# Kernel tuning notes

Measured on AMD Instinct MI355X. Metric: run time of the kernel, lower is better.

Reference implementation:

```python
import jax, jax.numpy as jnp
import numpy as np

# ---- module hyperparameters (match init_kwargs) ----
SPATIAL = (32, 64)          # token grid, N = 32*64 = 2048
D_MODEL = 1024
N_HEADS = 16
HEAD_DIM = D_MODEL // N_HEADS  # 64
THETA = 10000.0
XPOS_SCALE_BASE = SPATIAL[0] * 2  # 64


def _rope_tables():
    """ND rotary (xpos) tables, lucidrains-style.
    Each spatial axis gets head_dim//ndim rotary channels; frequencies are
    interleave-repeated (r=2) to pair with rotate_half. Returns cos, sin,
    xpos scale, each [N, HEAD_DIM] float32."""
    nd = len(SPATIAL)
    dpa = HEAD_DIM // nd  # dims per axis (32)
    freqs_axes, scale_axes = [], []
    for size in SPATIAL:
        inv_freq = 1.0 / (THETA ** (np.arange(0, dpa, 2, dtype=np.float64) / dpa))
        t = np.arange(size, dtype=np.float64)
        f = np.repeat(t[:, None] * inv_freq[None, :], 2, axis=-1)        # [size, dpa]
        sbase = (np.arange(0, dpa, 2, dtype=np.float64) + 0.4 * dpa) / (1.4 * dpa)
        power = (t - size // 2) / XPOS_SCALE_BASE
        sc = np.repeat(sbase[None, :] ** power[:, None], 2, axis=-1)     # [size, dpa]
        freqs_axes.append(f)
        scale_axes.append(sc)
    # broadcast each axis table over the full grid, concat along channel dim
    def grid_concat(tabs):
        parts = []
        for i, tab in enumerate(tabs):
            shp = [1] * nd + [dpa]
            shp[i] = SPATIAL[i]
            parts.append(np.broadcast_to(tab.reshape(shp), tuple(SPATIAL) + (dpa,)))
        return np.concatenate(parts, axis=-1).reshape(-1, HEAD_DIM)  # [N, HEAD_DIM]
    freqs = grid_concat(freqs_axes)
    xscale = grid_concat(scale_axes)
    return (jnp.asarray(np.cos(freqs), jnp.float32),
            jnp.asarray(np.sin(freqs), jnp.float32),
            jnp.asarray(xscale, jnp.float32))


def _rotate_half(x):
    # pairwise rotation: (x1, x2) -> (-x2, x1), interleaved layout
    x = x.reshape(*x.shape[:-1], -1, 2)
    x1, x2 = x[..., 0], x[..., 1]
    return jnp.stack((-x2, x1), axis=-1).reshape(*x.shape[:-2], -1)


def setup_inputs() -> dict:
    key = jax.random.key(0)
    ks = jax.random.split(key, 3)
    B, N = 2, SPATIAL[0] * SPATIAL[1]
    x = jax.random.normal(ks[0], (B, N, D_MODEL), dtype=jnp.float32)
    w_qkv = jax.random.normal(ks[1], (D_MODEL, 3 * D_MODEL), dtype=jnp.float32) * 0.02
    b_qkv = jnp.zeros((3 * D_MODEL,), jnp.float32)
    w_proj = jax.random.normal(ks[2], (D_MODEL, D_MODEL), dtype=jnp.float32) * 0.02
    b_proj = jnp.zeros((D_MODEL,), jnp.float32)
    return {"x": x, "w_qkv": w_qkv, "b_qkv": b_qkv, "w_proj": w_proj, "b_proj": b_proj}


def reference(x, w_qkv, b_qkv, w_proj, b_proj):
    B, N, C = x.shape
    scale = HEAD_DIM ** -0.5
    qkv = (x @ w_qkv + b_qkv).reshape(B, N, 3, N_HEADS, HEAD_DIM)
    qkv = qkv.transpose(2, 0, 3, 1, 4)  # [3, B, H, N, D]
    q, k, v = qkv[0], qkv[1], qkv[2]
    cos, sin, xs = _rope_tables()       # [N, D], broadcast over B,H
    q = (q * cos + _rotate_half(q) * sin) * xs
    k = (k * cos + _rotate_half(k) * sin) / xs
    attn = jax.nn.softmax(jnp.einsum('bhnd,bhmd->bhnm', q, k) * scale, axis=-1)
    out = jnp.einsum('bhnm,bhmd->bhnd', attn, v)
    out = out.transpose(0, 2, 1, 3).reshape(B, N, C)
    return out @ w_proj + b_proj
```

## Files before the change

kernel.cpp:

```cpp
#include <hip/hip_runtime.h>
#include <math.h>

typedef __attribute__((ext_vector_type(8))) _Float16 f16x8;
typedef __attribute__((ext_vector_type(4))) _Float16 f16x4;
typedef __attribute__((ext_vector_type(4))) float f32x4;

#define MFMAH(a, b, c) __builtin_amdgcn_mfma_f32_16x16x32_f16((a), (b), (c), 0, 0, 0)

#define QSCALE 0.18033688011112042f
#define SOFF 4.328085122666891f


__global__ void prep_kernel(const float* __restrict__ x, const float* __restrict__ w_qkv,
                            const float* __restrict__ w_proj, _Float16* __restrict__ xb,
                            _Float16* __restrict__ wq, _Float16* __restrict__ wp,
                            float* __restrict__ ct, float* __restrict__ st,
                            float* __restrict__ xt) {
    const int b = blockIdx.x, tid = threadIdx.x;
    if (b < 16384) {
        int i = b * 256 + tid;
        xb[i] = (_Float16)x[i];
    } else if (b < 28672) {
        int i = (b - 16384) * 256 + tid;
        int c = i >> 10, r = i & 1023;
        wq[i] = (_Float16)w_qkv[(size_t)r * 3072 + c];
    } else if (b < 32768) {
        int i = (b - 28672) * 256 + tid;
        int c = i >> 10, r = i & 1023;
        wp[i] = (_Float16)w_proj[(size_t)r * 1024 + c];
    } else {
        int i = (b - 32768) * 256 + tid;
        int n = i >> 6, d = i & 63;
        int gi = n >> 6, gj = n & 63;
        int axis = d >> 5;
        int p = (d & 31) >> 1;
        float t = axis ? (float)gj : (float)gi;
        float half = axis ? 32.0f : 16.0f;
        float inv_freq = powf(10000.0f, -(float)p * (1.0f / 16.0f));
        float fr = t * inv_freq;
        float sbase = (2.0f * p + 12.8f) / 44.8f;
        float xs = powf(sbase, (t - half) * (1.0f / 64.0f));
        ct[i] = cosf(fr);
        st[i] = sinf(fr);
        xt[i] = xs;
    }
}

#define LDK 40

__global__ __launch_bounds__(256) void gemm_qkv_kernel(
    const _Float16* __restrict__ A_g, const _Float16* __restrict__ B_g,
    const float* __restrict__ bias, const float* __restrict__ ctab,
    const float* __restrict__ stab, const float* __restrict__ xtab,
    _Float16* __restrict__ qb, _Float16* __restrict__ kb, _Float16* __restrict__ vt) {
    __shared__ __align__(16) _Float16 Asm[128 * LDK];
    __shared__ __align__(16) _Float16 Bsm[128 * LDK];

    const int tid = threadIdx.x;
    const int lane = tid & 63, wave = tid >> 6;
    const int quad = lane >> 4, l16 = lane & 15;
    const int wm = wave >> 1, wn = wave & 1;
    const int m0 = blockIdx.x * 128, n0 = blockIdx.y * 128;

    f32x4 zero = {0.f, 0.f, 0.f, 0.f};
    f32x4 acc[4][4];
#pragma unroll
    for (int i = 0; i < 4; ++i)
#pragma unroll
        for (int j = 0; j < 4; ++j) acc[i][j] = zero;

    const int r0 = tid >> 2, o0 = (tid & 3) << 3;
    const size_t ab = (size_t)m0 * 1024;
    const size_t bb = (size_t)n0 * 1024;

    f16x8 pa0 = *(const f16x8*)&A_g[ab + (size_t)r0 * 1024 + o0];
    f16x8 pa1 = *(const f16x8*)&A_g[ab + (size_t)(r0 + 64) * 1024 + o0];
    f16x8 pb0 = *(const f16x8*)&B_g[bb + (size_t)r0 * 1024 + o0];
    f16x8 pb1 = *(const f16x8*)&B_g[bb + (size_t)(r0 + 64) * 1024 + o0];

    for (int k0 = 0; k0 < 1024; k0 += 32) {
        __syncthreads();
        *(f16x8*)&Asm[r0 * LDK + o0] = pa0;
        *(f16x8*)&Asm[(r0 + 64) * LDK + o0] = pa1;
        *(f16x8*)&Bsm[r0 * LDK + o0] = pb0;
        *(f16x8*)&Bsm[(r0 + 64) * LDK + o0] = pb1;
        __syncthreads();

        if (k0 + 32 < 1024) {
            const int kn = k0 + 32;
            pa0 = *(const f16x8*)&A_g[ab + kn + (size_t)r0 * 1024 + o0];
            pa1 = *(const f16x8*)&A_g[ab + kn + (size_t)(r0 + 64) * 1024 + o0];
            pb0 = *(const f16x8*)&B_g[bb + kn + (size_t)r0 * 1024 + o0];
            pb1 = *(const f16x8*)&B_g[bb + kn + (size_t)(r0 + 64) * 1024 + o0];
        }

        f16x8 af[4], bf[4];
#pragma unroll
        for (int i = 0; i < 4; ++i) {
            af[i] = *(const f16x8*)&Asm[(wm * 64 + i * 16 + l16) * LDK + quad * 8];
            bf[i] = *(const f16x8*)&Bsm[(wn * 64 + i * 16 + l16) * LDK + quad * 8];
        }
#pragma unroll
        for (int i = 0; i < 4; ++i)
#pragma unroll
            for (int j = 0; j < 4; ++j) acc[i][j] = MFMAH(af[i], bf[j], acc[i][j]);
    }

    float bj[4];
#pragma unroll
    for (int j = 0; j < 4; ++j) bj[j] = bias[n0 + wn * 64 + j * 16 + l16];

    if (n0 < 2048) {
#pragma unroll
        for (int i = 0; i < 4; ++i) {
#pragma unroll
            for (int r = 0; r < 4; ++r) {
                const int row = m0 + wm * 64 + i * 16 + quad * 4 + r;
                const int b = row >> 11, nrow = row & 2047;
#pragma unroll
                for (int j = 0; j < 4; ++j) {
                    const int col = n0 + wn * 64 + j * 16 + l16;
                    float v = acc[i][j][r] + bj[j];
                    float partner = __shfl_xor(v, 1);
                    const int hh = (col >> 6) & 15;
                    const int d = col & 63;
                    const size_t o = ((size_t)(b * 16 + hh) * 2048 + nrow) * 64 + d;
                    float rh = (d & 1) ? partner : -partner;
                    const int ti = nrow * 64 + d;
                    float rv = v * ctab[ti] + rh * stab[ti];
                    float xs = xtab[ti];
                    if (col < 1024)
                        qb[o] = (_Float16)(rv * xs * QSCALE);
                    else
                        kb[o] = (_Float16)(rv / xs);
                }
            }
        }
    } else {
#pragma unroll
        for (int i = 0; i < 4; ++i) {
            const int row = m0 + wm * 64 + i * 16 + quad * 4;
            const int b = row >> 11, nrow = row & 2047;
#pragma unroll
            for (int j = 0; j < 4; ++j) {
                const int col = n0 + wn * 64 + j * 16 + l16;
                const int hh = (col >> 6) & 15;
                const int d = col & 63;
                f16x4 pv4;
#pragma unroll
                for (int r = 0; r < 4; ++r) pv4[r] = (_Float16)(acc[i][j][r] + bj[j]);
                *(f16x4*)&vt[((size_t)(b * 16 + hh) * 64 + d) * 2048 + nrow] = pv4;
            }
        }
    }
}

__global__ __launch_bounds__(256) void gemm_proj_kernel(
    const _Float16* __restrict__ A_g, const _Float16* __restrict__ B_g,
    const float* __restrict__ bias, float* __restrict__ out) {
    __shared__ __align__(16) _Float16 Asm[128 * LDK];
    __shared__ __align__(16) _Float16 Bsm[64 * LDK];

    const int tid = threadIdx.x;
    const int lane = tid & 63, wave = tid >> 6;
    const int quad = lane >> 4, l16 = lane & 15;
    const int wm = wave >> 1, wn = wave & 1;
    const int m0 = blockIdx.x * 128, n0 = blockIdx.y * 64;

    f32x4 zero = {0.f, 0.f, 0.f, 0.f};
    f32x4 acc[4][2];
#pragma unroll
    for (int i = 0; i < 4; ++i)
#pragma unroll
        for (int j = 0; j < 2; ++j) acc[i][j] = zero;

    const int r0 = tid >> 2, o0 = (tid & 3) << 3;
    const size_t ab = (size_t)m0 * 1024;
    const size_t bb = (size_t)n0 * 1024;

    f16x8 pa0 = *(const f16x8*)&A_g[ab + (size_t)r0 * 1024 + o0];
    f16x8 pa1 = *(const f16x8*)&A_g[ab + (size_t)(r0 + 64) * 1024 + o0];
    f16x8 pb0 = *(const f16x8*)&B_g[bb + (size_t)r0 * 1024 + o0];

    for (int k0 = 0; k0 < 1024; k0 += 32) {
        __syncthreads();
        *(f16x8*)&Asm[r0 * LDK + o0] = pa0;
        *(f16x8*)&Asm[(r0 + 64) * LDK + o0] = pa1;
        *(f16x8*)&Bsm[r0 * LDK + o0] = pb0;
        __syncthreads();

        if (k0 + 32 < 1024) {
            const int kn = k0 + 32;
            pa0 = *(const f16x8*)&A_g[ab + kn + (size_t)r0 * 1024 + o0];
            pa1 = *(const f16x8*)&A_g[ab + kn + (size_t)(r0 + 64) * 1024 + o0];
            pb0 = *(const f16x8*)&B_g[bb + kn + (size_t)r0 * 1024 + o0];
        }

        f16x8 af[4], bf[2];
#pragma unroll
        for (int i = 0; i < 4; ++i)
            af[i] = *(const f16x8*)&Asm[(wm * 64 + i * 16 + l16) * LDK + quad * 8];
#pragma unroll
        for (int j = 0; j < 2; ++j)
            bf[j] = *(const f16x8*)&Bsm[(wn * 32 + j * 16 + l16) * LDK + quad * 8];
#pragma unroll
        for (int i = 0; i < 4; ++i)
#pragma unroll
            for (int j = 0; j < 2; ++j) acc[i][j] = MFMAH(af[i], bf[j], acc[i][j]);
    }

    float bj[2];
#pragma unroll
    for (int j = 0; j < 2; ++j) bj[j] = bias[n0 + wn * 32 + j * 16 + l16];
#pragma unroll
    for (int i = 0; i < 4; ++i)
#pragma unroll
        for (int r = 0; r < 4; ++r) {
            const int row = m0 + wm * 64 + i * 16 + quad * 4 + r;
#pragma unroll
            for (int j = 0; j < 2; ++j) {
                const int col = n0 + wn * 32 + j * 16 + l16;
                out[(size_t)row * 1024 + col] = acc[i][j][r] + bj[j];
            }
        }
}

#define KLD 72
#define PLD 72

__global__ __launch_bounds__(256) void attn_kernel(
    const _Float16* __restrict__ qb, const _Float16* __restrict__ kb,
    const _Float16* __restrict__ vt, _Float16* __restrict__ ao) {
    __shared__ __align__(16) _Float16 Ksm0[64 * KLD], Ksm1[64 * KLD];
    __shared__ __align__(16) _Float16 Vsm0[64 * KLD], Vsm1[64 * KLD];
    __shared__ __align__(16) _Float16 Psm[4 * 32 * PLD];

    const int tid = threadIdx.x;
    const int lane = tid & 63, wave = tid >> 6;
    const int quad = lane >> 4, l16 = lane & 15;
    const int bh = blockIdx.x & 31, qt = blockIdx.x >> 5;
    const size_t base = (size_t)bh * 2048 * 64;
    const int qrow0 = qt * 128 + wave * 32;

    f16x8 qf[2][2];
#pragma unroll
    for (int rg = 0; rg < 2; ++rg) {
        qf[rg][0] = *(const f16x8*)&qb[base + (size_t)(qrow0 + rg * 16 + l16) * 64 + quad * 8];
        qf[rg][1] = *(const f16x8*)&qb[base + (size_t)(qrow0 + rg * 16 + l16) * 64 + 32 + quad * 8];
    }

    f32x4 moff = {-SOFF, -SOFF, -SOFF, -SOFF};
    f32x4 zero = {0.f, 0.f, 0.f, 0.f};
    f32x4 o[2][4];
    float lsum[2] = {0.f, 0.f};
#pragma unroll
    for (int rg = 0; rg < 2; ++rg)
#pragma unroll
        for (int dc = 0; dc < 4; ++dc) o[rg][dc] = zero;

    const int kr0 = tid >> 3, ko0 = (tid & 7) << 3;
    const int kr1 = kr0 + 32;
    f16x8 pk0, pk1, pv0, pv1;
    auto gload = [&](int kt) {
        pk0 = *(const f16x8*)&kb[base + (size_t)(kt + kr0) * 64 + ko0];
        pk1 = *(const f16x8*)&kb[base + (size_t)(kt + kr1) * 64 + ko0];
        pv0 = *(const f16x8*)&vt[((size_t)bh * 64 + kr0) * 2048 + kt + ko0];
        pv1 = *(const f16x8*)&vt[((size_t)bh * 64 + kr1) * 2048 + kt + ko0];
    };
    auto stage = [&](_Float16* Ks, _Float16* Vs) {
        *(f16x8*)&Ks[kr0 * KLD + ko0] = pk0;
        *(f16x8*)&Ks[kr1 * KLD + ko0] = pk1;
        *(f16x8*)&Vs[kr0 * KLD + ko0] = pv0;
        *(f16x8*)&Vs[kr1 * KLD + ko0] = pv1;
    };

    _Float16* Pw = &Psm[wave * 32 * PLD];

    auto compute = [&](const _Float16* Ks, const _Float16* Vs) {
        f32x4 s[2][4];
#pragma unroll
        for (int kg = 0; kg < 4; ++kg) {
            f16x8 kf0 = *(const f16x8*)&Ks[(kg * 16 + l16) * KLD + quad * 8];
            f16x8 kf1 = *(const f16x8*)&Ks[(kg * 16 + l16) * KLD + 32 + quad * 8];
            s[0][kg] = MFMAH(kf0, qf[0][0], moff);
            s[0][kg] = MFMAH(kf1, qf[0][1], s[0][kg]);
            s[1][kg] = MFMAH(kf0, qf[1][0], moff);
            s[1][kg] = MFMAH(kf1, qf[1][1], s[1][kg]);
        }
#pragma unroll
        for (int rg = 0; rg < 2; ++rg)
#pragma unroll
            for (int kg = 0; kg < 4; ++kg) {
                float p0 = __builtin_amdgcn_exp2f(s[rg][kg][0]);
                float p1 = __builtin_amdgcn_exp2f(s[rg][kg][1]);
                float p2 = __builtin_amdgcn_exp2f(s[rg][kg][2]);
                float p3 = __builtin_amdgcn_exp2f(s[rg][kg][3]);
                lsum[rg] += (p0 + p1) + (p2 + p3);
                f16x4 ph = {(_Float16)p0, (_Float16)p1, (_Float16)p2, (_Float16)p3};
                *(f16x4*)&Pw[(rg * 16 + l16) * PLD + kg * 16 + quad * 4] = ph;
            }
        f16x8 pf[2][2];
#pragma unroll
        for (int rg = 0; rg < 2; ++rg) {
            pf[rg][0] = *(const f16x8*)&Pw[(rg * 16 + l16) * PLD + quad * 8];
            pf[rg][1] = *(const f16x8*)&Pw[(rg * 16 + l16) * PLD + 32 + quad * 8];
        }
#pragma unroll
        for (int dc = 0; dc < 4; ++dc) {
            f16x8 vf0 = *(const f16x8*)&Vs[(dc * 16 + l16) * KLD + quad * 8];
            f16x8 vf1 = *(const f16x8*)&Vs[(dc * 16 + l16) * KLD + 32 + quad * 8];
#pragma unroll
            for (int rg = 0; rg < 2; ++rg) {
                o[rg][dc] = MFMAH(pf[rg][0], vf0, o[rg][dc]);
                o[rg][dc] = MFMAH(pf[rg][1], vf1, o[rg][dc]);
            }
        }
    };

    gload(0);
    stage(Ksm0, Vsm0);
    gload(64);
    __syncthreads();

    for (int it = 0; it < 32; it += 2) {
        stage(Ksm1, Vsm1);
        if (it + 2 < 32) gload((it + 2) * 64);
        compute(Ksm0, Vsm0);
        __syncthreads();
        if (it + 2 < 32) stage(Ksm0, Vsm0);
        if (it + 3 < 32) gload((it + 3) * 64);
        compute(Ksm1, Vsm1);
        __syncthreads();
    }

    float linv[2][4];
#pragma unroll
    for (int rg = 0; rg < 2; ++rg) {
        float v = lsum[rg];
        v += __shfl_xor(v, 16);
        v += __shfl_xor(v, 32);
        v = 1.0f / v;
#pragma unroll
        for (int r = 0; r < 4; ++r) linv[rg][r] = __shfl(v, quad * 4 + r);
    }

    const int b = bh >> 4, hh = bh & 15;
#pragma unroll
    for (int rg = 0; rg < 2; ++rg)
#pragma unroll
        for (int dc = 0; dc < 4; ++dc)
#pragma unroll
            for (int r = 0; r < 4; ++r) {
                float v = o[rg][dc][r] * linv[rg][r];
                const int qrow = qrow0 + rg * 16 + quad * 4 + r;
                const size_t oi = ((size_t)(b * 2048 + qrow)) * 1024 + hh * 64 + dc * 16 + l16;
                ao[oi] = (_Float16)v;
            }
}

extern "C" void kernel_launch(void* const* d_in, const int* in_sizes, int n_in,
                              void* d_out, int out_size, void* d_ws, size_t ws_size,
                              hipStream_t stream) {
    const float* x = (const float*)d_in[0];
    const float* w_qkv = (const float*)d_in[1];
    const float* b_qkv = (const float*)d_in[2];
    const float* w_proj = (const float*)d_in[3];
    const float* b_proj = (const float*)d_in[4];
    float* out = (float*)d_out;

    char* ws = (char*)d_ws;
    size_t off = 0;
    auto take = [&](size_t bytes) { char* p = ws + off; off += bytes; return p; };
    _Float16* xbuf   = (_Float16*)take(8388608);
    _Float16* wqkvT  = (_Float16*)take(6291456);
    _Float16* wprojT = (_Float16*)take(2097152);
    _Float16* qbuf   = (_Float16*)take(8388608);
    _Float16* kbuf   = (_Float16*)take(8388608);
    _Float16* vtbuf  = (_Float16*)take(8388608);
    float* ctab      = (float*)take(524288);
    float* stab      = (float*)take(524288);
    float* xtab      = (float*)take(524288);
    _Float16* ao = xbuf;

    prep_kernel<<<33280, 256, 0, stream>>>(x, w_qkv, w_proj, xbuf, wqkvT, wprojT,
                                           ctab, stab, xtab);
    gemm_qkv_kernel<<<dim3(32, 24), 256, 0, stream>>>(xbuf, wqkvT, b_qkv,
                                                      ctab, stab, xtab, qbuf, kbuf, vtbuf);
    attn_kernel<<<512, 256, 0, stream>>>(qbuf, kbuf, vtbuf, ao);
    gemm_proj_kernel<<<dim3(32, 16), 256, 0, stream>>>(ao, wprojT, b_proj, out);
}
```

Measured before the change: 219.3 us.

## Vectorize prep casts, tile weight transposes via LDS, use MFMA-ordered LDS layout

The prep kernel now converts x with float4 loads and f16x4 stores and transposes the weights through a padded 32x33 shared tile, so both global reads and writes are coalesced where the old strided gather was not. The two GEMM kernels change their LDS staging layout to a fragment-contiguous order: each thread stores its 16-byte chunk at tid*8 and each MFMA fragment is read as one contiguous 512-element block. This drops the padded row stride and aims to remove bank conflicts and address arithmetic. The trade-off is that global loads into LDS now follow a row/k interleave that may coalesce less well.

```diff
diff --git a/kernel.cpp b/kernel.cpp
--- a/kernel.cpp
+++ b/kernel.cpp
@@ -16,20 +16,34 @@
                             _Float16* __restrict__ wq, _Float16* __restrict__ wp,
                             float* __restrict__ ct, float* __restrict__ st,
                             float* __restrict__ xt) {
+    __shared__ float tile[32][33];
     const int b = blockIdx.x, tid = threadIdx.x;
-    if (b < 16384) {
-        int i = b * 256 + tid;
-        xb[i] = (_Float16)x[i];
-    } else if (b < 28672) {
-        int i = (b - 16384) * 256 + tid;
-        int c = i >> 10, r = i & 1023;
-        wq[i] = (_Float16)w_qkv[(size_t)r * 3072 + c];
-    } else if (b < 32768) {
-        int i = (b - 28672) * 256 + tid;
-        int c = i >> 10, r = i & 1023;
-        wp[i] = (_Float16)w_proj[(size_t)r * 1024 + c];
+    if (b < 4096) {
+        int i = (b * 256 + tid) * 4;
+        float4 v = *(const float4*)&x[i];
+        f16x4 h = {(_Float16)v.x, (_Float16)v.y, (_Float16)v.z, (_Float16)v.w};
+        *(f16x4*)&xb[i] = h;
+    } else if (b < 4096 + 3072 + 1024) {
+        int t, C;
+        const float* src;
+        _Float16* dst;
+        if (b < 4096 + 3072) { t = b - 4096; C = 3072; src = w_qkv; dst = wq; }
+        else                 { t = b - 4096 - 3072; C = 1024; src = w_proj; dst = wp; }
+        const int tr = t & 31, tc = t >> 5;
+        const int tx = tid & 31, ty = tid >> 5;
+#pragma unroll
+        for (int yy = 0; yy < 4; ++yy) {
+            int r = ty + yy * 8;
+            tile[r][tx] = src[(size_t)(tr * 32 + r) * C + tc * 32 + tx];
+        }
+        __syncthreads();
+#pragma unroll
+        for (int yy = 0; yy < 4; ++yy) {
+            int r = ty + yy * 8;
+            dst[(size_t)(tc * 32 + r) * 1024 + tr * 32 + tx] = (_Float16)tile[tx][r];
+        }
     } else {
-        int i = (b - 32768) * 256 + tid;
+        int i = (b - 8192) * 256 + tid;
         int n = i >> 6, d = i & 63;
         int gi = n >> 6, gj = n & 63;
         int axis = d >> 5;
@@ -46,15 +60,13 @@
     }
 }
 
-#define LDK 40
-
 __global__ __launch_bounds__(256) void gemm_qkv_kernel(
     const _Float16* __restrict__ A_g, const _Float16* __restrict__ B_g,
     const float* __restrict__ bias, const float* __restrict__ ctab,
     const float* __restrict__ stab, const float* __restrict__ xtab,
     _Float16* __restrict__ qb, _Float16* __restrict__ kb, _Float16* __restrict__ vt) {
-    __shared__ __align__(16) _Float16 Asm[128 * LDK];
-    __shared__ __align__(16) _Float16 Bsm[128 * LDK];
+    __shared__ __align__(16) _Float16 Asm[4096];
+    __shared__ __align__(16) _Float16 Bsm[4096];
 
     const int tid = threadIdx.x;
     const int lane = tid & 63, wave = tid >> 6;
@@ -69,36 +81,40 @@
 #pragma unroll
         for (int j = 0; j < 4; ++j) acc[i][j] = zero;
 
-    const int r0 = tid >> 2, o0 = (tid & 3) << 3;
-    const size_t ab = (size_t)m0 * 1024;
-    const size_t bb = (size_t)n0 * 1024;
-
-    f16x8 pa0 = *(const f16x8*)&A_g[ab + (size_t)r0 * 1024 + o0];
-    f16x8 pa1 = *(const f16x8*)&A_g[ab + (size_t)(r0 + 64) * 1024 + o0];
-    f16x8 pb0 = *(const f16x8*)&B_g[bb + (size_t)r0 * 1024 + o0];
-    f16x8 pb1 = *(const f16x8*)&B_g[bb + (size_t)(r0 + 64) * 1024 + o0];
+    const int c1 = tid + 256;
+    const int row0 = ((tid >> 6) << 4) | (tid & 15), ko0 = ((tid >> 4) & 3) << 3;
+    const int row1 = ((c1 >> 6) << 4) | (c1 & 15), ko1 = ((c1 >> 4) & 3) << 3;
+    const _Float16* Ap0 = &A_g[(size_t)(m0 + row0) * 1024 + ko0];
+    const _Float16* Ap1 = &A_g[(size_t)(m0 + row1) * 1024 + ko1];
+    const _Float16* Bp0 = &B_g[(size_t)(n0 + row0) * 1024 + ko0];
+    const _Float16* Bp1 = &B_g[(size_t)(n0 + row1) * 1024 + ko1];
+
+    f16x8 pa0 = *(const f16x8*)Ap0;
+    f16x8 pa1 = *(const f16x8*)Ap1;
+    f16x8 pb0 = *(const f16x8*)Bp0;
+    f16x8 pb1 = *(const f16x8*)Bp1;
 
     for (int k0 = 0; k0 < 1024; k0 += 32) {
         __syncthreads();
-        *(f16x8*)&Asm[r0 * LDK + o0] = pa0;
-        *(f16x8*)&Asm[(r0 + 64) * LDK + o0] = pa1;
-        *(f16x8*)&Bsm[r0 * LDK + o0] = pb0;
-        *(f16x8*)&Bsm[(r0 + 64) * LDK + o0] = pb1;
+        *(f16x8*)&Asm[tid * 8] = pa0;
+        *(f16x8*)&Asm[c1 * 8] = pa1;
+        *(f16x8*)&Bsm[tid * 8] = pb0;
+        *(f16x8*)&Bsm[c1 * 8] = pb1;
         __syncthreads();
 
         if (k0 + 32 < 1024) {
             const int kn = k0 + 32;
-            pa0 = *(const f16x8*)&A_g[ab + kn + (size_t)r0 * 1024 + o0];
-            pa1 = *(const f16x8*)&A_g[ab + kn + (size_t)(r0 + 64) * 1024 + o0];
-            pb0 = *(const f16x8*)&B_g[bb + kn + (size_t)r0 * 1024 + o0];
-            pb1 = *(const f16x8*)&B_g[bb + kn + (size_t)(r0 + 64) * 1024 + o0];
+            pa0 = *(const f16x8*)(Ap0 + kn);
+            pa1 = *(const f16x8*)(Ap1 + kn);
+            pb0 = *(const f16x8*)(Bp0 + kn);
+            pb1 = *(const f16x8*)(Bp1 + kn);
         }
 
         f16x8 af[4], bf[4];
 #pragma unroll
         for (int i = 0; i < 4; ++i) {
-            af[i] = *(const f16x8*)&Asm[(wm * 64 + i * 16 + l16) * LDK + quad * 8];
-            bf[i] = *(const f16x8*)&Bsm[(wn * 64 + i * 16 + l16) * LDK + quad * 8];
+            af[i] = *(const f16x8*)&Asm[(wm * 4 + i) * 512 + quad * 128 + l16 * 8];
+            bf[i] = *(const f16x8*)&Bsm[(wn * 4 + i) * 512 + quad * 128 + l16 * 8];
         }
 #pragma unroll
         for (int i = 0; i < 4; ++i)
@@ -158,8 +174,8 @@
 __global__ __launch_bounds__(256) void gemm_proj_kernel(
     const _Float16* __restrict__ A_g, const _Float16* __restrict__ B_g,
     const float* __restrict__ bias, float* __restrict__ out) {
-    __shared__ __align__(16) _Float16 Asm[128 * LDK];
-    __shared__ __align__(16) _Float16 Bsm[64 * LDK];
+    __shared__ __align__(16) _Float16 Asm[4096];
+    __shared__ __align__(16) _Float16 Bsm[2048];
 
     const int tid = threadIdx.x;
     const int lane = tid & 63, wave = tid >> 6;
@@ -174,35 +190,38 @@
 #pragma unroll
         for (int j = 0; j < 2; ++j) acc[i][j] = zero;
 
-    const int r0 = tid >> 2, o0 = (tid & 3) << 3;
-    const size_t ab = (size_t)m0 * 1024;
-    const size_t bb = (size_t)n0 * 1024;
-
-    f16x8 pa0 = *(const f16x8*)&A_g[ab + (size_t)r0 * 1024 + o0];
-    f16x8 pa1 = *(const f16x8*)&A_g[ab + (size_t)(r0 + 64) * 1024 + o0];
-    f16x8 pb0 = *(const f16x8*)&B_g[bb + (size_t)r0 * 1024 + o0];
+    const int c1 = tid + 256;
+    const int row0 = ((tid >> 6) << 4) | (tid & 15), ko0 = ((tid >> 4) & 3) << 3;
+    const int row1 = ((c1 >> 6) << 4) | (c1 & 15), ko1 = ((c1 >> 4) & 3) << 3;
+    const _Float16* Ap0 = &A_g[(size_t)(m0 + row0) * 1024 + ko0];
+    const _Float16* Ap1 = &A_g[(size_t)(m0 + row1) * 1024 + ko1];
+    const _Float16* Bp0 = &B_g[(size_t)(n0 + row0) * 1024 + ko0];
+
+    f16x8 pa0 = *(const f16x8*)Ap0;
+    f16x8 pa1 = *(const f16x8*)Ap1;
+    f16x8 pb0 = *(const f16x8*)Bp0;
 
     for (int k0 = 0; k0 < 1024; k0 += 32) {
         __syncthreads();
-        *(f16x8*)&Asm[r0 * LDK + o0] = pa0;
-        *(f16x8*)&Asm[(r0 + 64) * LDK + o0] = pa1;
-        *(f16x8*)&Bsm[r0 * LDK + o0] = pb0;
+        *(f16x8*)&Asm[tid * 8] = pa0;
+        *(f16x8*)&Asm[c1 * 8] = pa1;
+        *(f16x8*)&Bsm[tid * 8] = pb0;
         __syncthreads();
 
         if (k0 + 32 < 1024) {
             const int kn = k0 + 32;
-            pa0 = *(const f16x8*)&A_g[ab + kn + (size_t)r0 * 1024 + o0];
-            pa1 = *(const f16x8*)&A_g[ab + kn + (size_t)(r0 + 64) * 1024 + o0];
-            pb0 = *(const f16x8*)&B_g[bb + kn + (size_t)r0 * 1024 + o0];
+            pa0 = *(const f16x8*)(Ap0 + kn);
+            pa1 = *(const f16x8*)(Ap1 + kn);
+            pb0 = *(const f16x8*)(Bp0 + kn);
         }
 
         f16x8 af[4], bf[2];
 #pragma unroll
         for (int i = 0; i < 4; ++i)
-            af[i] = *(const f16x8*)&Asm[(wm * 64 + i * 16 + l16) * LDK + quad * 8];
+            af[i] = *(const f16x8*)&Asm[(wm * 4 + i) * 512 + quad * 128 + l16 * 8];
 #pragma unroll
         for (int j = 0; j < 2; ++j)
-            bf[j] = *(const f16x8*)&Bsm[(wn * 32 + j * 16 + l16) * LDK + quad * 8];
+            bf[j] = *(const f16x8*)&Bsm[(wn * 2 + j) * 512 + quad * 128 + l16 * 8];
 #pragma unroll
         for (int i = 0; i < 4; ++i)
 #pragma unroll
@@ -382,8 +401,8 @@
     float* xtab      = (float*)take(524288);
     _Float16* ao = xbuf;
 
-    prep_kernel<<<33280, 256, 0, stream>>>(x, w_qkv, w_proj, xbuf, wqkvT, wprojT,
-                                           ctab, stab, xtab);
+    prep_kernel<<<8704, 256, 0, stream>>>(x, w_qkv, w_proj, xbuf, wqkvT, wprojT,
+                                          ctab, stab, xtab);
     gemm_qkv_kernel<<<dim3(32, 24), 256, 0, stream>>>(xbuf, wqkvT, b_qkv,
                                                       ctab, stab, xtab, qbuf, kbuf, vtbuf);
     attn_kernel<<<512, 256, 0, stream>>>(qbuf, kbuf, vtbuf, ao);
```

Result: slower. 228.5 us (+4.2%).
